# Performance work log

Measured on AMD Instinct MI355X. Metric: run time of the kernel, lower is better.

Reference implementation:

```python
import jax, jax.numpy as jnp
import numpy as np

B, N, M, D, H = 2, 2048, 2048, 1024, 16
HD = D // H          # head_dim = 64
F = int(D * 4.0)     # mlp hidden = 4096
EPS = 1e-5


def layernorm(x, w, b):
    mu = jnp.mean(x, axis=-1, keepdims=True)
    var = jnp.mean(jnp.square(x - mu), axis=-1, keepdims=True)
    return (x - mu) * jax.lax.rsqrt(var + EPS) * w + b


def setup_inputs() -> dict:
    key = jax.random.key(0)
    ks = jax.random.split(key, 8)
    w = lambda k, shape: jax.random.normal(k, shape, dtype=jnp.float32) * 0.02
    return {
        "query": jax.random.normal(ks[0], (B, N, D), dtype=jnp.float32),
        "context": jax.random.normal(ks[1], (B, M, D), dtype=jnp.float32),
        "qpos": jax.random.randint(ks[2], (B, N), 0, N, dtype=jnp.int32),
        "cpos": jax.random.randint(ks[3], (B, M), 0, M, dtype=jnp.int32),
        "Wq_w": w(ks[4], (D, D)), "Wq_b": jnp.zeros((D,), jnp.float32),
        "Wk_w": w(ks[5], (D, D)), "Wk_b": jnp.zeros((D,), jnp.float32),
        "Wv_w": w(ks[6], (D, D)), "Wv_b": jnp.zeros((D,), jnp.float32),
        "qn_w": jnp.ones((HD,), jnp.float32), "qn_b": jnp.zeros((HD,), jnp.float32),
        "kn_w": jnp.ones((HD,), jnp.float32), "kn_b": jnp.zeros((HD,), jnp.float32),
        "ffn_w": jnp.ones((D,), jnp.float32), "ffn_b": jnp.zeros((D,), jnp.float32),
        "fc1_w": w(ks[7], (D, F)), "fc1_b": jnp.zeros((F,), jnp.float32),
        "fc2_w": w(jax.random.fold_in(key, 99), (F, D)), "fc2_b": jnp.zeros((D,), jnp.float32),
    }


def reference(query, context, qpos, cpos,
              Wq_w, Wq_b, Wk_w, Wk_b, Wv_w, Wv_b,
              qn_w, qn_b, kn_w, kn_b,
              ffn_w, ffn_b, fc1_w, fc1_b, fc2_w, fc2_b):
    # rope=None -> qpos/cpos unused (kept for signature fidelity)
    res = query
    # QKV projections, split heads -> (B,H,T,HD)
    Q = (query @ Wq_w + Wq_b).reshape(B, N, H, HD).transpose(0, 2, 1, 3)
    K = (context @ Wk_w + Wk_b).reshape(B, M, H, HD).transpose(0, 2, 1, 3)
    V = (context @ Wv_w + Wv_b).reshape(B, M, H, HD).transpose(0, 2, 1, 3)
    # per-head LayerNorm on q and k
    Q = layernorm(Q, qn_w, qn_b)
    K = layernorm(K, kn_w, kn_b)
    # attention
    scores = jnp.einsum('bhnd,bhmd->bhnm', Q, K) / jnp.sqrt(jnp.float32(HD))
    attn = jax.nn.softmax(scores, axis=-1)
    out = jnp.einsum('bhnm,bhmd->bhnd', attn, V)
    out = out.transpose(0, 2, 1, 3).reshape(B, N, D)
    out = res + out
    # MLP block with pre-norm
    res2 = out
    h = layernorm(out, ffn_w, ffn_b)
    h = jax.nn.gelu(h @ fc1_w + fc1_b, approximate=False)
    h = h @ fc2_w + fc2_b
    return res2 + h
```

## Files before the change

### kernel.cpp

```cpp
#include <hip/hip_runtime.h>
#include <hip/hip_bf16.h>
#include <math.h>

constexpr int Bb  = 2;
constexpr int Nn  = 2048;
constexpr int Mm  = 2048;
constexpr int Dd  = 1024;
constexpr int Hh  = 16;
constexpr int HD  = 64;
constexpr int Ff  = 4096;
constexpr float EPS = 1e-5f;
constexpr float QSCALE = 0.125f * 1.4426950408889634f;
constexpr float SMAX = 12.0f;

typedef __attribute__((ext_vector_type(8))) short bf16x8;
typedef __attribute__((ext_vector_type(4))) short bf16x4;
typedef __attribute__((ext_vector_type(4))) float f32x4;

__device__ inline unsigned short f2bf(float f) {
    __hip_bfloat16 h = __float2bfloat16(f);
    return *reinterpret_cast<unsigned short*>(&h);
}
__device__ inline unsigned short f2bf_rh(float f) {
    union { float f; unsigned u; } c{f};
    return (unsigned short)((c.u + 0x8000u) >> 16);
}
__device__ inline float bf2f(unsigned short u) {
    union { unsigned u; float f; } c{(unsigned)u << 16};
    return c.f;
}

__device__ inline float gelu_fast(float x) {
    float t = x * x;
    float f = fmaf(-0.10295004f, t, -2.30211782f);
    float e = __builtin_amdgcn_exp2f(x * f);
    return x * __builtin_amdgcn_rcpf(1.0f + e);
}

__device__ inline void async_load16(const void* g, void* l) {
    __builtin_amdgcn_global_load_lds(
        (const __attribute__((address_space(1))) void*)g,
        (__attribute__((address_space(3))) void*)l, 16, 0, 0);
}

__device__ inline bf16x8 ld_b64x2(const unsigned short* p) {
    bf16x4 lo = *(const bf16x4*)p;
    bf16x4 hi = *(const bf16x4*)(p + 4);
    bf16x8 r;
#pragma unroll
    for (int i = 0; i < 4; i++) { r[i] = lo[i]; r[i + 4] = hi[i]; }
    return r;
}

__global__ __launch_bounds__(256) void prep_kernel(
    const float* __restrict__ query, const float* __restrict__ context,
    unsigned short* __restrict__ qa, unsigned short* __restrict__ ca,
    const float* __restrict__ W0, const float* __restrict__ W1,
    const float* __restrict__ W2, const float* __restrict__ W3,
    const float* __restrict__ W4,
    unsigned short* __restrict__ T0, unsigned short* __restrict__ T1,
    unsigned short* __restrict__ T2, unsigned short* __restrict__ T3,
    unsigned short* __restrict__ T4)
{
    __shared__ float tile[32][33];
    int bid = blockIdx.x;
    if (bid < 8192) {
        int i = bid * 256 + threadIdx.x;
        const float* x; unsigned short* y; int k;
        if (i < 1048576) { x = query; y = qa; k = i; }
        else { x = context; y = ca; k = i - 1048576; }
        float4 v = reinterpret_cast<const float4*>(x)[k];
        ushort4 o;
        o.x = f2bf(v.x); o.y = f2bf(v.y); o.z = f2bf(v.z); o.w = f2bf(v.w);
        reinterpret_cast<ushort4*>(y)[k] = o;
        return;
    }
    bid -= 8192;
    const float* W; unsigned short* T; int K, Cn, tid;
    if (bid < 3072) {
        int j = bid >> 10; tid = bid & 1023;
        W = (j == 0) ? W0 : (j == 1) ? W1 : W2;
        T = (j == 0) ? T0 : (j == 1) ? T1 : T2;
        K = Dd; Cn = Dd;
    } else if (bid < 7168) {
        tid = bid - 3072; W = W3; T = T3; K = Dd; Cn = Ff;
    } else {
        tid = bid - 7168; W = W4; T = T4; K = Ff; Cn = Dd;
    }
    int xt = Cn >> 5;
    int bx = tid % xt, by = tid / xt;
    int tx = threadIdx.x & 31, ty = threadIdx.x >> 5;
    int c = bx * 32 + tx;
    int kbase = by * 32;
#pragma unroll
    for (int i = ty; i < 32; i += 8)
        tile[i][tx] = W[(size_t)(kbase + i) * Cn + c];
    __syncthreads();
    int k = kbase + tx;
#pragma unroll
    for (int i = ty; i < 32; i += 8)
        T[(size_t)(bx * 32 + i) * K + k] = f2bf(tile[tx][i]);
}

__global__ __launch_bounds__(256) void qkv_fused_kernel(
    const unsigned short* __restrict__ qa, const unsigned short* __restrict__ ca,
    const unsigned short* __restrict__ Wqt, const unsigned short* __restrict__ Wkt,
    const unsigned short* __restrict__ Wvt,
    const float* __restrict__ bq, const float* __restrict__ bk,
    const float* __restrict__ bv,
    const float* __restrict__ qn_w, const float* __restrict__ qn_b,
    const float* __restrict__ kn_w, const float* __restrict__ kn_b,
    unsigned short* __restrict__ Qbh, unsigned short* __restrict__ Kbh,
    unsigned short* __restrict__ Vt_g)
{
    __shared__ __align__(16) unsigned short As[2][128 * 32];
    __shared__ __align__(16) unsigned short Bs[2][128 * 32];

    const int bz = blockIdx.z;
    const unsigned short* A  = (bz == 0) ? qa : ca;
    const unsigned short* Bt = (bz == 0) ? Wqt : (bz == 1) ? Wkt : Wvt;
    const float* bias        = (bz == 0) ? bq  : (bz == 1) ? bk  : bv;
    const int K = Dd;

    const int t    = threadIdx.x;
    const int wave = t >> 6;
    const int lane = t & 63;
    const int r0 = blockIdx.y * 128;
    const int c0 = blockIdx.x * 128;
    const int wm = (wave >> 1) * 64;
    const int wn = (wave & 1) * 64;

    f32x4 acc[4][4];
#pragma unroll
    for (int i = 0; i < 4; i++)
#pragma unroll
        for (int j = 0; j < 4; j++) acc[i][j] = (f32x4)0.0f;

    const int row1 = t >> 2;
    const int kcs  = ((t & 3) ^ ((t >> 3) & 3)) * 8;
    const size_t arow1 = (size_t)(r0 + row1) * K + kcs;
    const size_t arow2 = (size_t)(r0 + row1 + 64) * K + kcs;
    const size_t brow1 = (size_t)(c0 + row1) * K + kcs;
    const size_t brow2 = (size_t)(c0 + row1 + 64) * K + kcs;
    char* A1_0 = (char*)&As[0][0] + wave * 1024;
    char* A2_0 = (char*)&As[0][0] + 4096 + wave * 1024;
    char* B1_0 = (char*)&Bs[0][0] + wave * 1024;
    char* B2_0 = (char*)&Bs[0][0] + 4096 + wave * 1024;
    char* A1_1 = (char*)&As[1][0] + wave * 1024;
    char* A2_1 = (char*)&As[1][0] + 4096 + wave * 1024;
    char* B1_1 = (char*)&Bs[1][0] + wave * 1024;
    char* B2_1 = (char*)&Bs[1][0] + 4096 + wave * 1024;

    const int m   = lane & 15;
    const int swc = ((lane >> 4) ^ ((m >> 1) & 3)) << 3;

    async_load16(A + arow1, A1_0);
    async_load16(A + arow2, A2_0);
    async_load16(Bt + brow1, B1_0);
    async_load16(Bt + brow2, B2_0);

    for (int k0 = 0; k0 < K; k0 += 32) {
        __syncthreads();
        const int cur = (k0 >> 5) & 1;
        if (k0 + 32 < K) {
            const int nk = k0 + 32;
            async_load16(A + arow1 + nk, cur ? A1_0 : A1_1);
            async_load16(A + arow2 + nk, cur ? A2_0 : A2_1);
            async_load16(Bt + brow1 + nk, cur ? B1_0 : B1_1);
            async_load16(Bt + brow2 + nk, cur ? B2_0 : B2_1);
        }
        const unsigned short* Ac = &As[cur][0];
        const unsigned short* Bc = &Bs[cur][0];

        bf16x8 af[4], bfr[4];
#pragma unroll
        for (int mi = 0; mi < 4; mi++)
            af[mi] = *(const bf16x8*)&Ac[(wm + mi * 16 + m) * 32 + swc];
#pragma unroll
        for (int nj = 0; nj < 4; nj++)
            bfr[nj] = *(const bf16x8*)&Bc[(wn + nj * 16 + m) * 32 + swc];
#pragma unroll
        for (int mi = 0; mi < 4; mi++)
#pragma unroll
            for (int nj = 0; nj < 4; nj++)
                acc[mi][nj] = __builtin_amdgcn_mfma_f32_16x16x32_bf16(
                    af[mi], bfr[nj], acc[mi][nj], 0, 0, 0);
    }

    const int rowb = r0 + wm + (lane >> 4) * 4;
    const int colb = c0 + wn + m;
#pragma unroll
    for (int nj = 0; nj < 4; nj++) {
        float bvv = bias[colb + nj * 16];
#pragma unroll
        for (int mi = 0; mi < 4; mi++)
#pragma unroll
            for (int r = 0; r < 4; r++) acc[mi][nj][r] += bvv;
    }

    if (bz < 2) {
        unsigned short* O = (bz == 0) ? Qbh : Kbh;
        const float* lw = (bz == 0) ? qn_w : kn_w;
        const float* lb = (bz == 0) ? qn_b : kn_b;
        const float scale = (bz == 0) ? QSCALE : 1.0f;
        const int hcol = c0 + wn;
        float w4[4], b4[4];
#pragma unroll
        for (int nj = 0; nj < 4; nj++) {
            int d = nj * 16 + m;
            w4[nj] = lw[d]; b4[nj] = lb[d];
        }
#pragma unroll
        for (int mi = 0; mi < 4; mi++) {
#pragma unroll
            for (int r = 0; r < 4; r++) {
                float s = (acc[mi][0][r] + acc[mi][1][r]) +
                          (acc[mi][2][r] + acc[mi][3][r]);
                s += __shfl_xor(s, 1); s += __shfl_xor(s, 2);
                s += __shfl_xor(s, 4); s += __shfl_xor(s, 8);
                float mu = s * (1.0f / 64.0f);
                float v2 = 0.f;
#pragma unroll
                for (int nj = 0; nj < 4; nj++) {
                    float dd = acc[mi][nj][r] - mu; v2 += dd * dd;
                }
                v2 += __shfl_xor(v2, 1); v2 += __shfl_xor(v2, 2);
                v2 += __shfl_xor(v2, 4); v2 += __shfl_xor(v2, 8);
                float rstd = rsqrtf(v2 * (1.0f / 64.0f) + EPS);
                size_t base = (size_t)(rowb + mi * 16 + r) * Dd + hcol;
#pragma unroll
                for (int nj = 0; nj < 4; nj++) {
                    int d = nj * 16 + m;
                    O[base + d] = f2bf(
                        ((acc[mi][nj][r] - mu) * rstd * w4[nj] + b4[nj]) * scale);
                }
            }
        }
    } else {
#pragma unroll
        for (int mi = 0; mi < 4; mi++) {
            int row0 = rowb + mi * 16;
            int bidx = row0 >> 11;
            int mtok = row0 & (Mm - 1);
#pragma unroll
            for (int nj = 0; nj < 4; nj++) {
                int col = colb + nj * 16;
                int h = col >> 6, d = col & 63;
                ushort4 o;
                o.x = f2bf(acc[mi][nj][0]);
                o.y = f2bf(acc[mi][nj][1]);
                o.z = f2bf(acc[mi][nj][2]);
                o.w = f2bf(acc[mi][nj][3]);
                *(ushort4*)(Vt_g + (((size_t)(bidx * Hh + h) * HD + d) << 11) + mtok) = o;
            }
        }
    }
}

template <int EPI, int OUTBF>
__global__ __launch_bounds__(256) void gemm_mfma_bt(
    const unsigned short* __restrict__ A,
    const unsigned short* __restrict__ Bt,
    const float* __restrict__ bias, const float* __restrict__ resid,
    void* __restrict__ Cout, int R, int K, int Cn)
{
    __shared__ __align__(16) unsigned short As[2][128 * 32];
    __shared__ __align__(16) unsigned short Bs[2][128 * 32];

    const int t    = threadIdx.x;
    const int wave = t >> 6;
    const int lane = t & 63;
    const int r0 = blockIdx.y * 128;
    const int c0 = blockIdx.x * 128;
    const int wm = (wave >> 1) * 64;
    const int wn = (wave & 1) * 64;

    f32x4 acc[4][4];
#pragma unroll
    for (int i = 0; i < 4; i++)
#pragma unroll
        for (int j = 0; j < 4; j++) acc[i][j] = (f32x4)0.0f;

    const int row1 = t >> 2;
    const int kcs  = ((t & 3) ^ ((t >> 3) & 3)) * 8;
    const size_t arow1 = (size_t)(r0 + row1) * K + kcs;
    const size_t arow2 = (size_t)(r0 + row1 + 64) * K + kcs;
    const size_t brow1 = (size_t)(c0 + row1) * K + kcs;
    const size_t brow2 = (size_t)(c0 + row1 + 64) * K + kcs;
    char* A1_0 = (char*)&As[0][0] + wave * 1024;
    char* A2_0 = (char*)&As[0][0] + 4096 + wave * 1024;
    char* B1_0 = (char*)&Bs[0][0] + wave * 1024;
    char* B2_0 = (char*)&Bs[0][0] + 4096 + wave * 1024;
    char* A1_1 = (char*)&As[1][0] + wave * 1024;
    char* A2_1 = (char*)&As[1][0] + 4096 + wave * 1024;
    char* B1_1 = (char*)&Bs[1][0] + wave * 1024;
    char* B2_1 = (char*)&Bs[1][0] + 4096 + wave * 1024;

    const int m   = lane & 15;
    const int swc = ((lane >> 4) ^ ((m >> 1) & 3)) << 3;

    async_load16(A + arow1, A1_0);
    async_load16(A + arow2, A2_0);
    async_load16(Bt + brow1, B1_0);
    async_load16(Bt + brow2, B2_0);

    for (int k0 = 0; k0 < K; k0 += 32) {
        __syncthreads();
        const int cur = (k0 >> 5) & 1;
        if (k0 + 32 < K) {
            const int nk = k0 + 32;
            async_load16(A + arow1 + nk, cur ? A1_0 : A1_1);
            async_load16(A + arow2 + nk, cur ? A2_0 : A2_1);
            async_load16(Bt + brow1 + nk, cur ? B1_0 : B1_1);
            async_load16(Bt + brow2 + nk, cur ? B2_0 : B2_1);
        }
        const unsigned short* Ac = &As[cur][0];
        const unsigned short* Bc = &Bs[cur][0];

        bf16x8 af[4], bfr[4];
#pragma unroll
        for (int mi = 0; mi < 4; mi++)
            af[mi] = *(const bf16x8*)&Ac[(wm + mi * 16 + m) * 32 + swc];
#pragma unroll
        for (int nj = 0; nj < 4; nj++)
            bfr[nj] = *(const bf16x8*)&Bc[(wn + nj * 16 + m) * 32 + swc];
#pragma unroll
        for (int mi = 0; mi < 4; mi++)
#pragma unroll
            for (int nj = 0; nj < 4; nj++)
                acc[mi][nj] = __builtin_amdgcn_mfma_f32_16x16x32_bf16(
                    af[mi], bfr[nj], acc[mi][nj], 0, 0, 0);
    }

    const int rowb = r0 + wm + (lane >> 4) * 4;
    const int colb = c0 + wn + m;
#pragma unroll
    for (int mi = 0; mi < 4; mi++) {
#pragma unroll
        for (int nj = 0; nj < 4; nj++) {
            int col = colb + nj * 16;
            float bv = bias[col];
#pragma unroll
            for (int r = 0; r < 4; r++) {
                int row = rowb + mi * 16 + r;
                float v = acc[mi][nj][r] + bv;
                if (EPI == 1) v = gelu_fast(v);
                if (resid) v += resid[(size_t)row * Cn + col];
                if (OUTBF)
                    ((unsigned short*)Cout)[(size_t)row * Cn + col] = f2bf(v);
                else
                    ((float*)Cout)[(size_t)row * Cn + col] = v;
            }
        }
    }
}

__global__ __launch_bounds__(256) void gemm_fc2_split(
    const unsigned short* __restrict__ A,
    const unsigned short* __restrict__ Bt,
    unsigned short* __restrict__ Part)
{
    constexpr int Kfull = Ff;
    constexpr int Ksub  = Ff / 4;
    constexpr int Cn    = Dd;
    const int split = blockIdx.z;
    const int koff  = split * Ksub;

    __shared__ __align__(16) unsigned short As[2][128 * 32];
    __shared__ __align__(16) unsigned short Bs[2][128 * 32];

    const int t    = threadIdx.x;
    const int wave = t >> 6;
    const int lane = t & 63;
    const int r0 = blockIdx.y * 128;
    const int c0 = blockIdx.x * 128;
    const int wm = (wave >> 1) * 64;
    const int wn = (wave & 1) * 64;

    f32x4 acc[4][4];
#pragma unroll
    for (int i = 0; i < 4; i++)
#pragma unroll
        for (int j = 0; j < 4; j++) acc[i][j] = (f32x4)0.0f;

    const int row1 = t >> 2;
    const int kcs  = ((t & 3) ^ ((t >> 3) & 3)) * 8;
    const size_t arow1 = (size_t)(r0 + row1) * Kfull + koff + kcs;
    const size_t arow2 = (size_t)(r0 + row1 + 64) * Kfull + koff + kcs;
    const size_t brow1 = (size_t)(c0 + row1) * Kfull + koff + kcs;
    const size_t brow2 = (size_t)(c0 + row1 + 64) * Kfull + koff + kcs;
    char* A1_0 = (char*)&As[0][0] + wave * 1024;
    char* A2_0 = (char*)&As[0][0] + 4096 + wave * 1024;
    char* B1_0 = (char*)&Bs[0][0] + wave * 1024;
    char* B2_0 = (char*)&Bs[0][0] + 4096 + wave * 1024;
    char* A1_1 = (char*)&As[1][0] + wave * 1024;
    char* A2_1 = (char*)&As[1][0] + 4096 + wave * 1024;
    char* B1_1 = (char*)&Bs[1][0] + wave * 1024;
    char* B2_1 = (char*)&Bs[1][0] + 4096 + wave * 1024;

    const int m   = lane & 15;
    const int swc = ((lane >> 4) ^ ((m >> 1) & 3)) << 3;

    async_load16(A + arow1, A1_0);
    async_load16(A + arow2, A2_0);
    async_load16(Bt + brow1, B1_0);
    async_load16(Bt + brow2, B2_0);

    for (int k0 = 0; k0 < Ksub; k0 += 32) {
        __syncthreads();
        const int cur = (k0 >> 5) & 1;
        if (k0 + 32 < Ksub) {
            const int nk = k0 + 32;
            async_load16(A + arow1 + nk, cur ? A1_0 : A1_1);
            async_load16(A + arow2 + nk, cur ? A2_0 : A2_1);
            async_load16(Bt + brow1 + nk, cur ? B1_0 : B1_1);
            async_load16(Bt + brow2 + nk, cur ? B2_0 : B2_1);
        }
        const unsigned short* Ac = &As[cur][0];
        const unsigned short* Bc = &Bs[cur][0];

        bf16x8 af[4], bfr[4];
#pragma unroll
        for (int mi = 0; mi < 4; mi++)
            af[mi] = *(const bf16x8*)&Ac[(wm + mi * 16 + m) * 32 + swc];
#pragma unroll
        for (int nj = 0; nj < 4; nj++)
            bfr[nj] = *(const bf16x8*)&Bc[(wn + nj * 16 + m) * 32 + swc];
#pragma unroll
        for (int mi = 0; mi < 4; mi++)
#pragma unroll
            for (int nj = 0; nj < 4; nj++)
                acc[mi][nj] = __builtin_amdgcn_mfma_f32_16x16x32_bf16(
                    af[mi], bfr[nj], acc[mi][nj], 0, 0, 0);
    }

    unsigned short* P = Part + (size_t)split * ((size_t)Bb * Nn * Dd);
    const int rowb = r0 + wm + (lane >> 4) * 4;
    const int colb = c0 + wn + m;
#pragma unroll
    for (int mi = 0; mi < 4; mi++)
#pragma unroll
        for (int nj = 0; nj < 4; nj++) {
            int col = colb + nj * 16;
#pragma unroll
            for (int r = 0; r < 4; r++)
                P[(size_t)(rowb + mi * 16 + r) * Cn + col] = f2bf(acc[mi][nj][r]);
        }
}

__global__ __launch_bounds__(256) void fc2_reduce_kernel(
    const unsigned short* __restrict__ Part, const float* __restrict__ bias,
    const float* __restrict__ attn, float* __restrict__ out)
{
    constexpr size_t NEl = (size_t)Bb * Nn * Dd;
    size_t i4 = (size_t)blockIdx.x * 256 + threadIdx.x;
    size_t i = i4 * 4;
    float4 s = *reinterpret_cast<const float4*>(attn + i);
    float4 bv = *reinterpret_cast<const float4*>(bias + (i & (Dd - 1)));
    s.x += bv.x; s.y += bv.y; s.z += bv.z; s.w += bv.w;
#pragma unroll
    for (int sp = 0; sp < 4; sp++) {
        ushort4 u = *reinterpret_cast<const ushort4*>(Part + sp * NEl + i);
        s.x += bf2f(u.x); s.y += bf2f(u.y); s.z += bf2f(u.z); s.w += bf2f(u.w);
    }
    *reinterpret_cast<float4*>(out + i) = s;
}

__global__ __launch_bounds__(256) void ln_row_bf16_kernel(
    const float* __restrict__ X, const float* __restrict__ w,
    const float* __restrict__ b, unsigned short* __restrict__ Y)
{
    int row = blockIdx.x;
    const float* x = X + (size_t)row * Dd;
    int t = threadIdx.x;
    float v[4];
    float s = 0.f;
#pragma unroll
    for (int i = 0; i < 4; i++) { v[i] = x[t + i * 256]; s += v[i]; }
#pragma unroll
    for (int off = 32; off; off >>= 1) s += __shfl_xor(s, off);
    __shared__ float red[4];
    __shared__ float stats[2];
    if ((t & 63) == 0) red[t >> 6] = s;
    __syncthreads();
    if (t == 0) stats[0] = (red[0] + red[1] + red[2] + red[3]) * (1.0f / Dd);
    __syncthreads();
    float mu = stats[0];
    float s2 = 0.f;
#pragma unroll
    for (int i = 0; i < 4; i++) { float d = v[i] - mu; s2 += d * d; }
#pragma unroll
    for (int off = 32; off; off >>= 1) s2 += __shfl_xor(s2, off);
    __syncthreads();
    if ((t & 63) == 0) red[t >> 6] = s2;
    __syncthreads();
    if (t == 0) stats[1] = (red[0] + red[1] + red[2] + red[3]) * (1.0f / Dd);
    __syncthreads();
    float rstd = rsqrtf(stats[1] + EPS);
    unsigned short* y = Y + (size_t)row * Dd;
#pragma unroll
    for (int i = 0; i < 4; i++) {
        int c = t + i * 256;
        y[c] = f2bf((v[i] - mu) * rstd * w[c] + b[c]);
    }
}

__global__ __launch_bounds__(512) void attention_mfma_kernel(
    const unsigned short* __restrict__ Qb,
    const unsigned short* __restrict__ Kb,
    const unsigned short* __restrict__ Vt_g,
    const float* __restrict__ query,
    float* __restrict__ Out)
{
    const int bid = blockIdx.x;
    const int g  = bid & 31;
    const int qt = bid >> 5;
    const int b  = g >> 4;
    const int h  = g & 15;
    const int q0 = qt * 128;

    __shared__ __align__(16) unsigned short Ks[2][2 * 64 * 32];
    __shared__ __align__(16) unsigned short Vts[2][2 * 64 * 32];
    __shared__ __align__(16) unsigned short Ps[8 * 16 * 68];

    const int t    = threadIdx.x;
    const int wave = t >> 6;
    const int lane = t & 63;
    const int m16  = lane & 15;
    const int kg   = lane >> 4;
    const int swc  = (kg ^ ((m16 >> 1) & 3)) << 3;

    bf16x8 qf[2];
    {
        const unsigned short* qp =
            Qb + ((size_t)(b * Nn + q0 + wave * 16 + m16) * Dd + h * HD + kg * 8);
        qf[0] = *(const bf16x8*)qp;
        qf[1] = *(const bf16x8*)(qp + 32);
    }

    f32x4 oacc[4];
    float lrow[4];
#pragma unroll
    for (int i = 0; i < 4; i++) { oacc[i] = (f32x4)0.f; lrow[i] = 0.f; }

    const size_t kbase  = (size_t)(b * Mm) * Dd + h * HD;
    const size_t vtbase = ((size_t)(b * Hh + h) * HD) * Mm;
    unsigned short* psw = Ps + wave * (16 * 68);

    const int u    = t & 255;
    const int pan  = t >> 8;
    const int srow = u >> 2;
    const int schk = ((u & 3) ^ ((srow >> 1) & 3)) * 8;
    char* kdstA = (char*)&Ks[0][0]  + pan * 4096 + (wave & 3) * 1024;
    char* kdstB = (char*)&Ks[1][0]  + pan * 4096 + (wave & 3) * 1024;
    char* vdstA = (char*)&Vts[0][0] + pan * 4096 + (wave & 3) * 1024;
    char* vdstB = (char*)&Vts[1][0] + pan * 4096 + (wave & 3) * 1024;
    const unsigned short* kp0 = Kb + kbase + (size_t)srow * Dd + schk + pan * 32;
    const unsigned short* vp0 = Vt_g + vtbase + (size_t)srow * Mm + schk + pan * 32;

    async_load16(kp0, kdstA);
    async_load16(vp0, vdstA);

    for (int m0 = 0; m0 < Mm; m0 += 64) {
        __syncthreads();
        const int cur = (m0 >> 6) & 1;
        if (m0 + 64 < Mm) {
            async_load16(kp0 + (size_t)(m0 + 64) * Dd, cur ? kdstA : kdstB);
            async_load16(vp0 + (m0 + 64),              cur ? vdstA : vdstB);
        }
        const unsigned short* Kc = &Ks[cur][0];
        const unsigned short* Vc = &Vts[cur][0];

        f32x4 s[4];
#pragma unroll
        for (int j = 0; j < 4; j++) {
            bf16x8 b0 = *(const bf16x8*)&Kc[(j * 16 + m16) * 32 + swc];
            bf16x8 b1 = *(const bf16x8*)&Kc[2048 + (j * 16 + m16) * 32 + swc];
            f32x4 a = (f32x4)(-SMAX);
            a = __builtin_amdgcn_mfma_f32_16x16x32_bf16(qf[0], b0, a, 0, 0, 0);
            a = __builtin_amdgcn_mfma_f32_16x16x32_bf16(qf[1], b1, a, 0, 0, 0);
            s[j] = a;
        }

#pragma unroll
        for (int r = 0; r < 4; r++) {
            float p0 = __builtin_amdgcn_exp2f(s[0][r]);
            float p1 = __builtin_amdgcn_exp2f(s[1][r]);
            float p2 = __builtin_amdgcn_exp2f(s[2][r]);
            float p3 = __builtin_amdgcn_exp2f(s[3][r]);
            lrow[r] += (p0 + p1) + (p2 + p3);
            int qrow = kg * 4 + r;
            psw[qrow * 68 +  0 + m16] = f2bf_rh(p0);
            psw[qrow * 68 + 16 + m16] = f2bf_rh(p1);
            psw[qrow * 68 + 32 + m16] = f2bf_rh(p2);
            psw[qrow * 68 + 48 + m16] = f2bf_rh(p3);
        }

        bf16x8 pf0 = ld_b64x2(psw + m16 * 68 + kg * 8);
        bf16x8 pf1 = ld_b64x2(psw + m16 * 68 + 32 + kg * 8);
#pragma unroll
        for (int dj = 0; dj < 4; dj++) {
            bf16x8 v0 = *(const bf16x8*)&Vc[(dj * 16 + m16) * 32 + swc];
            bf16x8 v1 = *(const bf16x8*)&Vc[2048 + (dj * 16 + m16) * 32 + swc];
            oacc[dj] = __builtin_amdgcn_mfma_f32_16x16x32_bf16(pf0, v0, oacc[dj], 0, 0, 0);
            oacc[dj] = __builtin_amdgcn_mfma_f32_16x16x32_bf16(pf1, v1, oacc[dj], 0, 0, 0);
        }
    }

#pragma unroll
    for (int r = 0; r < 4; r++) {
        float l = lrow[r];
        l += __shfl_xor(l, 1);
        l += __shfl_xor(l, 2);
        l += __shfl_xor(l, 4);
        l += __shfl_xor(l, 8);
        float inv = 1.0f / l;
        const size_t rowbase =
            (size_t)(b * Nn + q0 + wave * 16 + kg * 4 + r) * Dd + h * HD;
#pragma unroll
        for (int dj = 0; dj < 4; dj++) {
            size_t idx = rowbase + dj * 16 + m16;
            Out[idx] = query[idx] + oacc[dj][r] * inv;
        }
    }
}

extern "C" void kernel_launch(void* const* d_in, const int* in_sizes, int n_in,
                              void* d_out, int out_size, void* d_ws, size_t ws_size,
                              hipStream_t stream)
{
    const float* query   = (const float*)d_in[0];
    const float* context = (const float*)d_in[1];
    const float* Wq_w = (const float*)d_in[4];
    const float* Wq_b = (const float*)d_in[5];
    const float* Wk_w = (const float*)d_in[6];
    const float* Wk_b = (const float*)d_in[7];
    const float* Wv_w = (const float*)d_in[8];
    const float* Wv_b = (const float*)d_in[9];
    const float* qn_w = (const float*)d_in[10];
    const float* qn_b = (const float*)d_in[11];
    const float* kn_w = (const float*)d_in[12];
    const float* kn_b = (const float*)d_in[13];
    const float* ffn_w = (const float*)d_in[14];
    const float* ffn_b = (const float*)d_in[15];
    const float* fc1_w = (const float*)d_in[16];
    const float* fc1_b = (const float*)d_in[17];
    const float* fc2_w = (const float*)d_in[18];
    const float* fc2_b = (const float*)d_in[19];

    constexpr size_t BND = (size_t)Bb * Nn * Dd;
    constexpr size_t BMD = (size_t)Bb * Mm * Dd;
    constexpr size_t DD  = (size_t)Dd * Dd;
    constexpr size_t DF  = (size_t)Dd * Ff;

    const size_t need = BND * 4 + (2 * BND + 3 * BMD) * 2 + (3 * DD + 2 * DF) * 2
                      + 4 * BND * 2;
    if (ws_size < need) return;

    char* p = (char*)d_ws;
    float* attn = (float*)p;                   p += BND * 4;
    unsigned short* Qbh  = (unsigned short*)p; p += BND * 2;
    unsigned short* Kbh  = (unsigned short*)p; p += BMD * 2;
    unsigned short* Vt_g = (unsigned short*)p; p += BMD * 2;
    unsigned short* qa   = (unsigned short*)p; p += BND * 2;
    unsigned short* ca   = (unsigned short*)p; p += BMD * 2;
    unsigned short* Wqt  = (unsigned short*)p; p += DD * 2;
    unsigned short* Wkt  = (unsigned short*)p; p += DD * 2;
    unsigned short* Wvt  = (unsigned short*)p; p += DD * 2;
    unsigned short* fc1t = (unsigned short*)p; p += DF * 2;
    unsigned short* fc2t = (unsigned short*)p; p += DF * 2;
    unsigned short* part = (unsigned short*)p; p += 4 * BND * 2;
    unsigned short* normed = Qbh;
    unsigned short* mid    = Kbh;
    float* out = (float*)d_out;

    const int R = Bb * Nn;
    dim3 blk(256);

    prep_kernel<<<19456, blk, 0, stream>>>(
        query, context, qa, ca,
        Wq_w, Wk_w, Wv_w, fc1_w, fc2_w, Wqt, Wkt, Wvt, fc1t, fc2t);

    qkv_fused_kernel<<<dim3(Dd / 128, R / 128, 3), blk, 0, stream>>>(
        qa, ca, Wqt, Wkt, Wvt, Wq_b, Wk_b, Wv_b,
        qn_w, qn_b, kn_w, kn_b, Qbh, Kbh, Vt_g);

    attention_mfma_kernel<<<Bb * Hh * (Nn / 128), 512, 0, stream>>>(
        Qbh, Kbh, Vt_g, query, attn);

    ln_row_bf16_kernel<<<Bb * Nn, blk, 0, stream>>>(attn, ffn_w, ffn_b, normed);

    gemm_mfma_bt<1, 1><<<dim3(Ff / 128, R / 128), blk, 0, stream>>>(
        normed, fc1t, fc1_b, nullptr, mid, R, Dd, Ff);
    gemm_fc2_split<<<dim3(Dd / 128, R / 128, 4), blk, 0, stream>>>(
        mid, fc2t, part);
    fc2_reduce_kernel<<<BND / 4 / 256, blk, 0, stream>>>(
        part, fc2_b, attn, out);
}
```

Baseline: 367.3 us.

## Replace MLP GEMMs with 256x256-tile 8-wave phased pipelined MFMA kernel

Replaces the fc1 and fc2 split-K GEMMs, which used 128x128 tiles with K-step 32, with a single templated kernel. The new kernel uses 256x256 tiles, K-step 64, 512 threads, 128KB of dynamic LDS double buffering and grouped block ordering. Within each K-step it interleaves async global-to-LDS loads with four MFMA quadrants, using explicit vmcnt waits and barriers, to raise data reuse and overlap loads with compute. It also pads the attention P scratch rows from 68 to 72 so they can be read with single 128-bit LDS loads. Risks are fewer blocks (256) than CUs-times-occupancy, heavy register use, and fragile manual wait counts.

```diff
diff --git a/kernel.cpp b/kernel.cpp
--- a/kernel.cpp
+++ b/kernel.cpp
@@ -41,15 +41,6 @@
     __builtin_amdgcn_global_load_lds(
         (const __attribute__((address_space(1))) void*)g,
         (__attribute__((address_space(3))) void*)l, 16, 0, 0);
-}
-
-__device__ inline bf16x8 ld_b64x2(const unsigned short* p) {
-    bf16x4 lo = *(const bf16x4*)p;
-    bf16x4 hi = *(const bf16x4*)(p + 4);
-    bf16x8 r;
-#pragma unroll
-    for (int i = 0; i < 4; i++) { r[i] = lo[i]; r[i + 4] = hi[i]; }
-    return r;
 }
 
 __global__ __launch_bounds__(256) void prep_kernel(
@@ -257,195 +248,185 @@
     }
 }
 
-template <int EPI, int OUTBF>
-__global__ __launch_bounds__(256) void gemm_mfma_bt(
+#define QUAD(MH, BB, NH)                                                      \
+    {                                                                         \
+        _Pragma("unroll")                                                     \
+        for (int miq = 0; miq < 4; ++miq) {                                   \
+            _Pragma("unroll")                                                 \
+            for (int njq = 0; njq < 2; ++njq) {                               \
+                _Pragma("unroll")                                             \
+                for (int ks = 0; ks < 2; ++ks) {                              \
+                    acc[(MH) * 4 + miq][(NH) * 2 + njq] =                     \
+                        __builtin_amdgcn_mfma_f32_16x16x32_bf16(              \
+                            afr[miq][ks], BB[njq][ks],                        \
+                            acc[(MH) * 4 + miq][(NH) * 2 + njq], 0, 0, 0);    \
+                }                                                             \
+            }                                                                 \
+        }                                                                     \
+    }
+
+template <int MODE>
+__global__ __launch_bounds__(512, 2) void gemm_8ph(
     const unsigned short* __restrict__ A,
     const unsigned short* __restrict__ Bt,
-    const float* __restrict__ bias, const float* __restrict__ resid,
-    void* __restrict__ Cout, int R, int K, int Cn)
+    const float* __restrict__ bias,
+    unsigned short* __restrict__ Out)
 {
-    __shared__ __align__(16) unsigned short As[2][128 * 32];
-    __shared__ __align__(16) unsigned short Bs[2][128 * 32];
+    extern __shared__ char smem[];
+
+    constexpr int KstC = (MODE == 0) ? Dd : Ff;
+    constexpr int CnC  = (MODE == 0) ? Ff : Dd;
+    constexpr int NI   = 16;
+
+    const int chunk  = blockIdx.x & 7;
+    const int within = blockIdx.x >> 3;
+    int r0, c0, koff = 0;
+    if (MODE == 0) {
+        const int bx = (chunk & 3) * 4 + (within & 3);
+        const int by = (chunk >> 2) * 8 + (within >> 2);
+        r0 = by * 256; c0 = bx * 256;
+    } else {
+        const int split = chunk >> 1;
+        const int bx = within & 3;
+        const int by = (chunk & 1) * 8 + (within >> 2);
+        r0 = by * 256; c0 = bx * 256; koff = split * (Ff / 4);
+        Out += (size_t)split * ((size_t)Bb * Nn * Dd);
+    }
 
     const int t    = threadIdx.x;
     const int wave = t >> 6;
     const int lane = t & 63;
-    const int r0 = blockIdx.y * 128;
-    const int c0 = blockIdx.x * 128;
-    const int wm = (wave >> 1) * 64;
-    const int wn = (wave & 1) * 64;
-
-    f32x4 acc[4][4];
-#pragma unroll
-    for (int i = 0; i < 4; i++)
+    const int m16  = lane & 15;
+    const int kg4  = lane >> 4;
+    const int wr   = wave >> 2;
+    const int wc   = wave & 3;
+
+    const int u  = t >> 3;
+    const int cl = ((t & 7) ^ (u & 7)) * 8;
+    const unsigned short* sA0 = A + (size_t)(r0 + u) * KstC + koff + cl;
+    const unsigned short* sA1 = A + (size_t)(r0 + 128 + u) * KstC + koff + cl;
+    const int rB = (u & 31) + ((u >> 5) << 6);
+    const unsigned short* sB0 = Bt + (size_t)(c0 + rB) * KstC + koff + cl;
+    const unsigned short* sB1 = Bt + (size_t)(c0 + 128 + rB) * KstC + koff + cl;
+
+    int rdA[4], rdB[2], ck[2];
+#pragma unroll
+    for (int miq = 0; miq < 4; miq++) rdA[miq] = (wr * 64 + miq * 16 + m16) * 128;
+#pragma unroll
+    for (int njq = 0; njq < 2; njq++) rdB[njq] = (wc * 32 + njq * 16 + m16) * 128;
+#pragma unroll
+    for (int ks = 0; ks < 2; ks++) ck[ks] = (((ks * 4 + kg4) ^ (m16 & 7)) << 4);
+
+    f32x4 acc[8][4];
+#pragma unroll
+    for (int i = 0; i < 8; i++)
 #pragma unroll
         for (int j = 0; j < 4; j++) acc[i][j] = (f32x4)0.0f;
 
-    const int row1 = t >> 2;
-    const int kcs  = ((t & 3) ^ ((t >> 3) & 3)) * 8;
-    const size_t arow1 = (size_t)(r0 + row1) * K + kcs;
-    const size_t arow2 = (size_t)(r0 + row1 + 64) * K + kcs;
-    const size_t brow1 = (size_t)(c0 + row1) * K + kcs;
-    const size_t brow2 = (size_t)(c0 + row1 + 64) * K + kcs;
-    char* A1_0 = (char*)&As[0][0] + wave * 1024;
-    char* A2_0 = (char*)&As[0][0] + 4096 + wave * 1024;
-    char* B1_0 = (char*)&Bs[0][0] + wave * 1024;
-    char* B2_0 = (char*)&Bs[0][0] + 4096 + wave * 1024;
-    char* A1_1 = (char*)&As[1][0] + wave * 1024;
-    char* A2_1 = (char*)&As[1][0] + 4096 + wave * 1024;
-    char* B1_1 = (char*)&Bs[1][0] + wave * 1024;
-    char* B2_1 = (char*)&Bs[1][0] + 4096 + wave * 1024;
-
-    const int m   = lane & 15;
-    const int swc = ((lane >> 4) ^ ((m >> 1) & 3)) << 3;
-
-    async_load16(A + arow1, A1_0);
-    async_load16(A + arow2, A2_0);
-    async_load16(Bt + brow1, B1_0);
-    async_load16(Bt + brow2, B2_0);
-
-    for (int k0 = 0; k0 < K; k0 += 32) {
-        __syncthreads();
-        const int cur = (k0 >> 5) & 1;
-        if (k0 + 32 < K) {
-            const int nk = k0 + 32;
-            async_load16(A + arow1 + nk, cur ? A1_0 : A1_1);
-            async_load16(A + arow2 + nk, cur ? A2_0 : A2_1);
-            async_load16(Bt + brow1 + nk, cur ? B1_0 : B1_1);
-            async_load16(Bt + brow2 + nk, cur ? B2_0 : B2_1);
-        }
-        const unsigned short* Ac = &As[cur][0];
-        const unsigned short* Bc = &Bs[cur][0];
-
-        bf16x8 af[4], bfr[4];
-#pragma unroll
-        for (int mi = 0; mi < 4; mi++)
-            af[mi] = *(const bf16x8*)&Ac[(wm + mi * 16 + m) * 32 + swc];
-#pragma unroll
-        for (int nj = 0; nj < 4; nj++)
-            bfr[nj] = *(const bf16x8*)&Bc[(wn + nj * 16 + m) * 32 + swc];
-#pragma unroll
-        for (int mi = 0; mi < 4; mi++)
-#pragma unroll
-            for (int nj = 0; nj < 4; nj++)
-                acc[mi][nj] = __builtin_amdgcn_mfma_f32_16x16x32_bf16(
-                    af[mi], bfr[nj], acc[mi][nj], 0, 0, 0);
-    }
-
-    const int rowb = r0 + wm + (lane >> 4) * 4;
-    const int colb = c0 + wn + m;
-#pragma unroll
-    for (int mi = 0; mi < 4; mi++) {
-#pragma unroll
-        for (int nj = 0; nj < 4; nj++) {
-            int col = colb + nj * 16;
-            float bv = bias[col];
-#pragma unroll
-            for (int r = 0; r < 4; r++) {
-                int row = rowb + mi * 16 + r;
-                float v = acc[mi][nj][r] + bv;
-                if (EPI == 1) v = gelu_fast(v);
-                if (resid) v += resid[(size_t)row * Cn + col];
-                if (OUTBF)
-                    ((unsigned short*)Cout)[(size_t)row * Cn + col] = f2bf(v);
-                else
-                    ((float*)Cout)[(size_t)row * Cn + col] = v;
+    bf16x8 afr[4][2], b0r[2][2], b1r[2][2];
+
+    auto stA = [&](int mh, int nd, int kel) {
+        char* d = smem + nd * 65536 + mh * 16384 + wave * 1024;
+        async_load16(sA0 + (size_t)mh * 64 * KstC + kel, d);
+        async_load16(sA1 + (size_t)mh * 64 * KstC + kel, d + 8192);
+    };
+    auto stB = [&](int nh, int nd, int kel) {
+        char* d = smem + nd * 65536 + 32768 + nh * 16384 + wave * 1024;
+        async_load16(sB0 + (size_t)nh * 32 * KstC + kel, d);
+        async_load16(sB1 + (size_t)nh * 32 * KstC + kel, d + 8192);
+    };
+    auto ldA = [&](int cd, int mh) {
+        const char* base = smem + cd * 65536 + mh * 16384;
+#pragma unroll
+        for (int miq = 0; miq < 4; miq++)
+#pragma unroll
+            for (int ks = 0; ks < 2; ks++)
+                afr[miq][ks] = *(const bf16x8*)(base + rdA[miq] + ck[ks]);
+    };
+    auto ldB = [&](int cd, int nh, bf16x8 (&bb)[2][2]) {
+        const char* base = smem + cd * 65536 + 32768 + nh * 16384;
+#pragma unroll
+        for (int njq = 0; njq < 2; njq++)
+#pragma unroll
+            for (int ks = 0; ks < 2; ks++)
+                bb[njq][ks] = *(const bf16x8*)(base + rdB[njq] + ck[ks]);
+    };
+
+    stA(0, 0, 0); stB(0, 0, 0); stB(1, 0, 0); stA(1, 0, 0);
+    asm volatile("s_waitcnt vmcnt(0)" ::: "memory");
+    asm volatile("s_barrier" ::: "memory");
+
+    for (int it = 0; it < NI - 1; ++it) {
+        const int cd = it & 1, nd = cd ^ 1;
+        const int kn = (it + 1) * 64;
+        ldA(cd, 0); ldB(cd, 0, b0r);
+        stA(0, nd, kn);
+        asm volatile("s_waitcnt vmcnt(4)" ::: "memory");
+        asm volatile("s_barrier" ::: "memory");
+        QUAD(0, b0r, 0)
+        ldB(cd, 1, b1r);
+        stB(0, nd, kn);
+        asm volatile("s_waitcnt vmcnt(4)" ::: "memory");
+        asm volatile("s_barrier" ::: "memory");
+        QUAD(0, b1r, 1)
+        ldA(cd, 1);
+        stB(1, nd, kn);
+        asm volatile("s_barrier" ::: "memory");
+        QUAD(1, b1r, 1)
+        stA(1, nd, kn);
+        asm volatile("s_waitcnt vmcnt(4)" ::: "memory");
+        asm volatile("s_barrier" ::: "memory");
+        QUAD(1, b0r, 0)
+    }
+
+    {
+        const int cd = (NI - 1) & 1;
+        ldA(cd, 0); ldB(cd, 0, b0r);
+        asm volatile("s_waitcnt vmcnt(2)" ::: "memory");
+        asm volatile("s_barrier" ::: "memory");
+        QUAD(0, b0r, 0)
+        ldB(cd, 1, b1r);
+        asm volatile("s_waitcnt vmcnt(0)" ::: "memory");
+        asm volatile("s_barrier" ::: "memory");
+        QUAD(0, b1r, 1)
+        ldA(cd, 1);
+        QUAD(1, b1r, 1)
+        QUAD(1, b0r, 0)
+    }
+
+#pragma unroll
+    for (int MI = 0; MI < 8; MI++) {
+        const int row = r0 + wr * 128 + MI * 16 + kg4 * 4;
+#pragma unroll
+        for (int NJ = 0; NJ < 4; NJ++) {
+            const int col = c0 + wc * 64 + NJ * 16 + m16;
+            if (MODE == 0) {
+                const float bv = bias[col];
+#pragma unroll
+                for (int rr = 0; rr < 4; rr++) {
+                    float v = acc[MI][NJ][rr] + bv;
+                    v = gelu_fast(v);
+                    Out[(size_t)(row + rr) * CnC + col] = f2bf(v);
+                }
+            } else {
+#pragma unroll
+                for (int rr = 0; rr < 4; rr++)
+                    Out[(size_t)(row + rr) * CnC + col] = f2bf(acc[MI][NJ][rr]);
             }
         }
     }
 }
 
-__global__ __launch_bounds__(256) void gemm_fc2_split(
-    const unsigned short* __restrict__ A,
-    const unsigned short* __restrict__ Bt,
-    unsigned short* __restrict__ Part)
-{
-    constexpr int Kfull = Ff;
-    constexpr int Ksub  = Ff / 4;
-    constexpr int Cn    = Dd;
-    const int split = blockIdx.z;
-    const int koff  = split * Ksub;
-
-    __shared__ __align__(16) unsigned short As[2][128 * 32];
-    __shared__ __align__(16) unsigned short Bs[2][128 * 32];
-
-    const int t    = threadIdx.x;
-    const int wave = t >> 6;
-    const int lane = t & 63;
-    const int r0 = blockIdx.y * 128;
-    const int c0 = blockIdx.x * 128;
-    const int wm = (wave >> 1) * 64;
-    const int wn = (wave & 1) * 64;
-
-    f32x4 acc[4][4];
-#pragma unroll
-    for (int i = 0; i < 4; i++)
-#pragma unroll
-        for (int j = 0; j < 4; j++) acc[i][j] = (f32x4)0.0f;
-
-    const int row1 = t >> 2;
-    const int kcs  = ((t & 3) ^ ((t >> 3) & 3)) * 8;
-    const size_t arow1 = (size_t)(r0 + row1) * Kfull + koff + kcs;
-    const size_t arow2 = (size_t)(r0 + row1 + 64) * Kfull + koff + kcs;
-    const size_t brow1 = (size_t)(c0 + row1) * Kfull + koff + kcs;
-    const size_t brow2 = (size_t)(c0 + row1 + 64) * Kfull + koff + kcs;
-    char* A1_0 = (char*)&As[0][0] + wave * 1024;
-    char* A2_0 = (char*)&As[0][0] + 4096 + wave * 1024;
-    char* B1_0 = (char*)&Bs[0][0] + wave * 1024;
-    char* B2_0 = (char*)&Bs[0][0] + 4096 + wave * 1024;
-    char* A1_1 = (char*)&As[1][0] + wave * 1024;
-    char* A2_1 = (char*)&As[1][0] + 4096 + wave * 1024;
-    char* B1_1 = (char*)&Bs[1][0] + wave * 1024;
-    char* B2_1 = (char*)&Bs[1][0] + 4096 + wave * 1024;
-
-    const int m   = lane & 15;
-    const int swc = ((lane >> 4) ^ ((m >> 1) & 3)) << 3;
-
-    async_load16(A + arow1, A1_0);
-    async_load16(A + arow2, A2_0);
-    async_load16(Bt + brow1, B1_0);
-    async_load16(Bt + brow2, B2_0);
-
-    for (int k0 = 0; k0 < Ksub; k0 += 32) {
-        __syncthreads();
-        const int cur = (k0 >> 5) & 1;
-        if (k0 + 32 < Ksub) {
-            const int nk = k0 + 32;
-            async_load16(A + arow1 + nk, cur ? A1_0 : A1_1);
-            async_load16(A + arow2 + nk, cur ? A2_0 : A2_1);
-            async_load16(Bt + brow1 + nk, cur ? B1_0 : B1_1);
-            async_load16(Bt + brow2 + nk, cur ? B2_0 : B2_1);
-        }
-        const unsigned short* Ac = &As[cur][0];
-        const unsigned short* Bc = &Bs[cur][0];
-
-        bf16x8 af[4], bfr[4];
-#pragma unroll
-        for (int mi = 0; mi < 4; mi++)
-            af[mi] = *(const bf16x8*)&Ac[(wm + mi * 16 + m) * 32 + swc];
-#pragma unroll
-        for (int nj = 0; nj < 4; nj++)
-            bfr[nj] = *(const bf16x8*)&Bc[(wn + nj * 16 + m) * 32 + swc];
-#pragma unroll
-        for (int mi = 0; mi < 4; mi++)
-#pragma unroll
-            for (int nj = 0; nj < 4; nj++)
-                acc[mi][nj] = __builtin_amdgcn_mfma_f32_16x16x32_bf16(
-                    af[mi], bfr[nj], acc[mi][nj], 0, 0, 0);
-    }
-
-    unsigned short* P = Part + (size_t)split * ((size_t)Bb * Nn * Dd);
-    const int rowb = r0 + wm + (lane >> 4) * 4;
-    const int colb = c0 + wn + m;
-#pragma unroll
-    for (int mi = 0; mi < 4; mi++)
-#pragma unroll
-        for (int nj = 0; nj < 4; nj++) {
-            int col = colb + nj * 16;
-#pragma unroll
-            for (int r = 0; r < 4; r++)
-                P[(size_t)(rowb + mi * 16 + r) * Cn + col] = f2bf(acc[mi][nj][r]);
-        }
+namespace {
+struct Gemm8phAttrInit {
+    Gemm8phAttrInit() {
+        hipFuncSetAttribute(reinterpret_cast<const void*>(&gemm_8ph<0>),
+                            hipFuncAttributeMaxDynamicSharedMemorySize, 131072);
+        hipFuncSetAttribute(reinterpret_cast<const void*>(&gemm_8ph<1>),
+                            hipFuncAttributeMaxDynamicSharedMemorySize, 131072);
+    }
+};
+Gemm8phAttrInit g_gemm8ph_attr_init;
 }
 
 __global__ __launch_bounds__(256) void fc2_reduce_kernel(
@@ -521,7 +502,7 @@
 
     __shared__ __align__(16) unsigned short Ks[2][2 * 64 * 32];
     __shared__ __align__(16) unsigned short Vts[2][2 * 64 * 32];
-    __shared__ __align__(16) unsigned short Ps[8 * 16 * 68];
+    __shared__ __align__(16) unsigned short Ps[8 * 16 * 72];
 
     const int t    = threadIdx.x;
     const int wave = t >> 6;
@@ -545,7 +526,7 @@
 
     const size_t kbase  = (size_t)(b * Mm) * Dd + h * HD;
     const size_t vtbase = ((size_t)(b * Hh + h) * HD) * Mm;
-    unsigned short* psw = Ps + wave * (16 * 68);
+    unsigned short* psw = Ps + wave * (16 * 72);
 
     const int u    = t & 255;
     const int pan  = t >> 8;
@@ -590,14 +571,14 @@
             float p3 = __builtin_amdgcn_exp2f(s[3][r]);
             lrow[r] += (p0 + p1) + (p2 + p3);
             int qrow = kg * 4 + r;
-            psw[qrow * 68 +  0 + m16] = f2bf_rh(p0);
-            psw[qrow * 68 + 16 + m16] = f2bf_rh(p1);
-            psw[qrow * 68 + 32 + m16] = f2bf_rh(p2);
-            psw[qrow * 68 + 48 + m16] = f2bf_rh(p3);
-        }
-
-        bf16x8 pf0 = ld_b64x2(psw + m16 * 68 + kg * 8);
-        bf16x8 pf1 = ld_b64x2(psw + m16 * 68 + 32 + kg * 8);
+            psw[qrow * 72 +  0 + m16] = f2bf_rh(p0);
+            psw[qrow * 72 + 16 + m16] = f2bf_rh(p1);
+            psw[qrow * 72 + 32 + m16] = f2bf_rh(p2);
+            psw[qrow * 72 + 48 + m16] = f2bf_rh(p3);
+        }
+
+        bf16x8 pf0 = *(const bf16x8*)(psw + m16 * 72 + kg * 8);
+        bf16x8 pf1 = *(const bf16x8*)(psw + m16 * 72 + 32 + kg * 8);
 #pragma unroll
         for (int dj = 0; dj < 4; dj++) {
             bf16x8 v0 = *(const bf16x8*)&Vc[(dj * 16 + m16) * 32 + swc];
@@ -653,6 +634,15 @@
     constexpr size_t DD  = (size_t)Dd * Dd;
     constexpr size_t DF  = (size_t)Dd * Ff;
 
+    static bool attr_done = false;
+    if (!attr_done) {
+        hipFuncSetAttribute(reinterpret_cast<const void*>(&gemm_8ph<0>),
+                            hipFuncAttributeMaxDynamicSharedMemorySize, 131072);
+        hipFuncSetAttribute(reinterpret_cast<const void*>(&gemm_8ph<1>),
+                            hipFuncAttributeMaxDynamicSharedMemorySize, 131072);
+        attr_done = true;
+    }
+
     const size_t need = BND * 4 + (2 * BND + 3 * BMD) * 2 + (3 * DD + 2 * DF) * 2
                       + 4 * BND * 2;
     if (ws_size < need) return;
@@ -690,10 +680,8 @@
 
     ln_row_bf16_kernel<<<Bb * Nn, blk, 0, stream>>>(attn, ffn_w, ffn_b, normed);
 
-    gemm_mfma_bt<1, 1><<<dim3(Ff / 128, R / 128), blk, 0, stream>>>(
-        normed, fc1t, fc1_b, nullptr, mid, R, Dd, Ff);
-    gemm_fc2_split<<<dim3(Dd / 128, R / 128, 4), blk, 0, stream>>>(
-        mid, fc2t, part);
+    gemm_8ph<0><<<256, 512, 131072, stream>>>(normed, fc1t, fc1_b, mid);
+    gemm_8ph<1><<<256, 512, 131072, stream>>>(mid, fc2t, nullptr, part);
     fc2_reduce_kernel<<<BND / 4 / 256, blk, 0, stream>>>(
         part, fc2_b, attn, out);
 }
```

New measurement: 335.0 us. -8.8%, faster.
